# Optimization experiments

Measured on AMD Instinct MI355X. Metric: run time of the kernel, lower is better.

Reference implementation:

```python
import jax, jax.numpy as jnp
import numpy as np

D = 64       # hidden_dim
ED = 16      # edge_dim
N = 50000
E = 400000
T = 2
STEP = 0.5   # euler fixed step over t in [0,1] -> 2 steps
EPS = 1e-5

def setup_inputs() -> dict:
    key = jax.random.key(0)
    ks = jax.random.split(key, 14)
    def lin(k, fi, fo):
        return jax.random.normal(k, (fi, fo), jnp.float32) / np.sqrt(fi)
    return {
        'h_seq': jax.random.normal(ks[0], (T, N, D), jnp.float32),
        'edge_attr': jax.random.normal(ks[1], (T, E, ED), jnp.float32),
        # msg_net: MLP(2D+ED -> D -> D), 2 layers with ReLU
        'W1': lin(ks[2], 2 * D + ED, D), 'b1': jnp.zeros((D,), jnp.float32),
        'W2': lin(ks[3], D, D),          'b2': jnp.zeros((D,), jnp.float32),
        # dynamics_net: Linear(2D,D) -> LayerNorm -> SiLU -> Linear(D,D) -> Tanh
        'Wd1': lin(ks[4], 2 * D, D), 'bd1': jnp.zeros((D,), jnp.float32),
        'ln_g': jnp.ones((D,), jnp.float32), 'ln_b': jnp.zeros((D,), jnp.float32),
        'Wd2': lin(ks[5], D, D), 'bd2': jnp.zeros((D,), jnp.float32),
        'edge_index': jax.random.randint(ks[6], (T, 2, E), 0, N, jnp.int32),
    }

def _ode_func(h, row, col, ea, W1, b1, W2, b2, Wd1, bd1, ln_g, ln_b, Wd2, bd2):
    # identity transport: Q_uv @ h_v == h_v
    h_transported = h[col]                              # [E, D]
    msg_in = jnp.concatenate([h[row], h_transported, ea], axis=-1)  # [E, 2D+ED]
    msg = jax.nn.relu(msg_in @ W1 + b1) @ W2 + b2       # [E, D]
    agg = jax.ops.segment_sum(msg, row, num_segments=h.shape[0])    # [N, D]
    x = jnp.concatenate([h, agg], axis=-1) @ Wd1 + bd1  # [N, D]
    mu = x.mean(-1, keepdims=True)
    var = x.var(-1, keepdims=True)
    x = (x - mu) * jax.lax.rsqrt(var + EPS) * ln_g + ln_b
    x = jax.nn.silu(x) @ Wd2 + bd2
    return jnp.tanh(x)

def reference(h_seq, edge_attr, W1, b1, W2, b2, Wd1, bd1, ln_g, ln_b, Wd2, bd2, edge_index):
    params = (W1, b1, W2, b2, Wd1, bd1, ln_g, ln_b, Wd2, bd2)
    n_steps = int(round(1.0 / STEP))
    h_prev = h_seq[0]
    disagreements = []
    for t in range(T):
        row, col = edge_index[t, 0], edge_index[t, 1]
        ea = edge_attr[t]
        h = h_prev + h_seq[t]                           # h_fused
        for _ in range(n_steps):                        # fixed-step Euler
            h = h + STEP * _ode_func(h, row, col, ea, *params)
        diff = h[row] - h[col]                          # Q=I -> h_u - h_v
        disagreements.append(jnp.minimum((diff * diff).sum(-1), 1e4))
        h_prev = h
    return h_prev, jnp.stack(disagreements)             # h_final [N,D], D [T,E]
```

## Files before the change

kernel.cpp:

```cpp
#include <hip/hip_runtime.h>

#define NN 50000
#define EE 400000
#define NT64 6250
#define EGRID 1250
#define NBLK 782
#define SBLK 49

typedef __bf16 bf16x8 __attribute__((ext_vector_type(8)));
typedef float f32x4 __attribute__((ext_vector_type(4)));

static __device__ __forceinline__ ushort f2bf(float f) {
    union { float f; unsigned int i; } x; x.f = f;
    unsigned int r = x.i + 0x7fffu + ((x.i >> 16) & 1u);
    return (ushort)(r >> 16);
}
static __device__ __forceinline__ float bf2f(ushort u) {
    union { unsigned int i; float f; } x; x.i = ((unsigned int)u) << 16; return x.f;
}
static __device__ __forceinline__ unsigned pack2(float lo, float hi) {
    return (unsigned)f2bf(lo) | ((unsigned)f2bf(hi) << 16);
}
static __device__ __forceinline__ float fast_tanh(float x) {
    float e = __expf(2.f * x);
    return 1.f - 2.f / (e + 1.f);
}
static __device__ __forceinline__ bf16x8 pk8(float4 f0, float4 f1) {
    union { uint4 u; bf16x8 v; } z;
    z.u = make_uint4(pack2(f0.x, f0.y), pack2(f0.z, f0.w),
                     pack2(f1.x, f1.y), pack2(f1.z, f1.w));
    return z.v;
}
static __device__ __forceinline__ bf16x8 zero8() {
    union { uint4 u; bf16x8 v; } z;
    z.u = make_uint4(0u, 0u, 0u, 0u);
    return z.v;
}

__global__ __launch_bounds__(256) void prep_edge_k(
    const float* __restrict__ W1, const float* __restrict__ W2,
    const float* __restrict__ b1, const float* __restrict__ b2,
    ushort* __restrict__ B1P, ushort* __restrict__ B2P,
    float* __restrict__ b1f, float* __restrict__ b2f)
{
    int idx = blockIdx.x * 256 + threadIdx.x;
    if (idx < 10240) {
        int j = idx & 7, n = (idx >> 3) & 63, qk = idx >> 9;
        int kc = qk >> 2, quad = qk & 3;
        int k = kc * 32 + quad * 8 + j;
        B1P[idx] = (k < 144) ? f2bf(W1[k * 64 + n]) : (ushort)0;
    }
    if (idx < 4096) {
        int j = idx & 7, n = (idx >> 3) & 63, qk = idx >> 9;
        int kc = qk >> 2, quad = qk & 3;
        int k = kc * 32 + quad * 8 + j;
        B2P[idx] = f2bf(W2[k * 64 + n]);
    }
    if (idx < 64) { b1f[idx] = b1[idx]; b2f[idx] = b2[idx]; }
}

__global__ __launch_bounds__(256) void prep_node_k(
    const float* __restrict__ Wd1, const float* __restrict__ Wd2,
    const float* __restrict__ bd1, const float* __restrict__ lng,
    const float* __restrict__ lnb, const float* __restrict__ bd2,
    ushort* __restrict__ Wd1P, ushort* __restrict__ Wd2P,
    float* __restrict__ bd1f, float* __restrict__ lngf,
    float* __restrict__ lnbf, float* __restrict__ bd2f)
{
    int idx = blockIdx.x * 256 + threadIdx.x;
    if (idx < 8192) {
        int j = idx & 7, n = (idx >> 3) & 63, qk = idx >> 9;
        int kc = qk >> 2, quad = qk & 3;
        int k = kc * 32 + quad * 8 + j;
        Wd1P[idx] = f2bf(Wd1[k * 64 + n]);
    }
    if (idx < 4096) {
        int j = idx & 7, n = (idx >> 3) & 63, qk = idx >> 9;
        int kc = qk >> 2, quad = qk & 3;
        int k = kc * 32 + quad * 8 + j;
        Wd2P[idx] = f2bf(Wd2[k * 64 + n]);
    }
    if (idx < 64) {
        bd1f[idx] = bd1[idx]; lngf[idx] = lng[idx];
        lnbf[idx] = lnb[idx]; bd2f[idx] = bd2[idx];
    }
}

__global__ __launch_bounds__(256) void state_k(
    float* __restrict__ h, ushort* __restrict__ hb,
    const float* __restrict__ hseq_t, int mode)
{
    int i = blockIdx.x * 256 + threadIdx.x;
    float v = hseq_t[i];
    float r = (mode == 0) ? (2.f * v) : (h[i] + v);
    h[i] = r; hb[i] = f2bf(r);
}

__global__ __launch_bounds__(256) void zero_k(int* __restrict__ p, int n) {
    int i = blockIdx.x * 256 + threadIdx.x;
    if (i < n) p[i] = 0;
}
__global__ __launch_bounds__(256) void zero_f(float* __restrict__ p) {
    int i = blockIdx.x * 256 + threadIdx.x;
    p[i] = 0.f;
}
__global__ __launch_bounds__(256) void hist_k(const int* __restrict__ rows, int* __restrict__ counts) {
    int e = blockIdx.x * 256 + threadIdx.x;
    if (e < EE) atomicAdd(&counts[rows[e]], 1);
}

__global__ __launch_bounds__(256) void scanA_k(
    const int* __restrict__ counts, int* __restrict__ offsets, int* __restrict__ bsum)
{
    __shared__ int wsum[4];
    int tid = threadIdx.x, lane = tid & 63, w = tid >> 6;
    int i4 = blockIdx.x * 1024 + tid * 4;
    int4 v = make_int4(0, 0, 0, 0);
    if (i4 + 3 < NN) v = *(const int4*)(counts + i4);
    else {
        if (i4 < NN) v.x = counts[i4];
        if (i4 + 1 < NN) v.y = counts[i4 + 1];
        if (i4 + 2 < NN) v.z = counts[i4 + 2];
    }
    int s = v.x + v.y + v.z + v.w;
    int x = s;
    for (int off = 1; off < 64; off <<= 1) {
        int y = __shfl_up(x, off);
        if (lane >= off) x += y;
    }
    if (lane == 63) wsum[w] = x;
    __syncthreads();
    int wpre = 0;
    for (int j = 0; j < w; j++) wpre += wsum[j];
    int excl = wpre + x - s;
    int e0 = excl, e1 = e0 + v.x, e2 = e1 + v.y, e3 = e2 + v.z;
    if (i4 + 3 < NN) *(int4*)(offsets + i4) = make_int4(e0, e1, e2, e3);
    else {
        if (i4 < NN) offsets[i4] = e0;
        if (i4 + 1 < NN) offsets[i4 + 1] = e1;
        if (i4 + 2 < NN) offsets[i4 + 2] = e2;
    }
    if (tid == 255) bsum[blockIdx.x] = wpre + x;
}
__global__ __launch_bounds__(256) void scanC_k(
    const int* __restrict__ offsets, const int* __restrict__ bsum, int* __restrict__ cursor)
{
    int i = blockIdx.x * 256 + threadIdx.x;
    if (i < NN) {
        int b = i >> 10;
        int add = 0;
        for (int j = 0; j < b; j++) add += bsum[j];
        cursor[i] = offsets[i] + add;
    }
}

__global__ __launch_bounds__(256) void fill_idx_k(
    const int* __restrict__ rows, int* __restrict__ cursor, int* __restrict__ esort)
{
    int e = blockIdx.x * 256 + threadIdx.x;
    if (e < EE) {
        int p = atomicAdd(&cursor[rows[e]], 1);
        if ((unsigned)p < (unsigned)EE) esort[p] = e;
    }
}

__global__ __launch_bounds__(256) void gather_k(
    const int* __restrict__ esort, const int* __restrict__ rows,
    const int* __restrict__ cols, const float* __restrict__ ea,
    int* __restrict__ rsort, int* __restrict__ csort, ushort* __restrict__ eab)
{
    int p = blockIdx.x * 256 + threadIdx.x;
    if (p < EE) {
        int e = esort[p];
        rsort[p] = rows[e];
        csort[p] = cols[e];
        const float* sp = ea + (size_t)e * 16;
        float4 f0 = ((const float4*)sp)[0], f1 = ((const float4*)sp)[1];
        float4 f2 = ((const float4*)sp)[2], f3 = ((const float4*)sp)[3];
        uint4* dp = (uint4*)(eab + (size_t)p * 16);
        dp[0] = make_uint4(pack2(f0.x, f0.y), pack2(f0.z, f0.w),
                           pack2(f1.x, f1.y), pack2(f1.z, f1.w));
        dp[1] = make_uint4(pack2(f2.x, f2.y), pack2(f2.z, f2.w),
                           pack2(f3.x, f3.y), pack2(f3.z, f3.w));
    }
}

template<int MODE>
__global__ __launch_bounds__(256, 5) void edge_k(
    const ushort* __restrict__ hb,
    const int* __restrict__ ridx, const int* __restrict__ cidx,
    const ushort* __restrict__ eab, const float* __restrict__ eaf,
    const ushort* __restrict__ B1P, const ushort* __restrict__ B2P,
    const float* __restrict__ b1f, const float* __restrict__ b2f,
    float* __restrict__ agg)
{
    __shared__ __attribute__((aligned(16))) ushort sB1[10240];
    __shared__ __attribute__((aligned(16))) ushort sH[64 * 72];

    int tid = threadIdx.x;
    int lane = tid & 63, wave = tid >> 6;
    int m = lane & 15, quad = lane >> 4;

    for (int i = tid; i < 10240 / 8; i += 256) ((uint4*)sB1)[i] = ((const uint4*)B1P)[i];
    bf16x8 b2r[2][4];
    for (int kc = 0; kc < 2; kc++)
        for (int nt = 0; nt < 4; nt++)
            b2r[kc][nt] = *(const bf16x8*)(B2P + ((kc * 4 + quad) * 64 + nt * 16 + m) * 8);
    float b1v[4], b2v[4];
    for (int nt = 0; nt < 4; nt++) { b1v[nt] = b1f[nt * 16 + m]; b2v[nt] = b2f[nt * 16 + m]; }
    __syncthreads();

    ushort* sHw = sH + wave * 1152;
    int sl = wave * 16 + m;

    int t0 = blockIdx.x * 5;
    int r_n = ridx[t0 * 64 + sl], c_n = cidx[t0 * 64 + sl];

    for (int t = t0; t < t0 + 5; t++) {
        int s = t * 64 + sl;
        int r = r_n, c = c_n;

        bf16x8 a[5];
        a[0] = *(const bf16x8*)(hb + (size_t)r * 64 + quad * 8);
        a[1] = *(const bf16x8*)(hb + (size_t)r * 64 + 32 + quad * 8);
        a[2] = *(const bf16x8*)(hb + (size_t)c * 64 + quad * 8);
        a[3] = *(const bf16x8*)(hb + (size_t)c * 64 + 32 + quad * 8);
        a[4] = zero8();
        if (MODE == 0) {
            if (quad < 2) a[4] = *(const bf16x8*)(eab + (size_t)s * 16 + quad * 8);
        } else {
            if (quad < 2) {
                const float* sp = eaf + (size_t)s * 16 + quad * 8;
                float4 f0 = ((const float4*)sp)[0], f1 = ((const float4*)sp)[1];
                a[4] = pk8(f0, f1);
            }
        }

        int tn = t + 1; if (tn >= t0 + 5) tn = t;
        int sn = tn * 64 + sl;
        r_n = ridx[sn]; c_n = cidx[sn];

        f32x4 acc[4];
        #pragma unroll
        for (int nt = 0; nt < 4; nt++) acc[nt] = (f32x4){0.f, 0.f, 0.f, 0.f};
        #pragma unroll
        for (int kc = 0; kc < 5; kc++) {
            #pragma unroll
            for (int nt = 0; nt < 4; nt++) {
                bf16x8 b = *(const bf16x8*)(sB1 + ((kc * 4 + quad) * 64 + nt * 16 + m) * 8);
                acc[nt] = __builtin_amdgcn_mfma_f32_16x16x32_bf16(a[kc], b, acc[nt], 0, 0, 0);
            }
        }

        __builtin_amdgcn_wave_barrier();
        #pragma unroll
        for (int nt = 0; nt < 4; nt++) {
            int colid = nt * 16 + m;
            float bb = b1v[nt];
            #pragma unroll
            for (int rr = 0; rr < 4; rr++) {
                float v = acc[nt][rr] + bb;
                v = v > 0.f ? v : 0.f;
                sHw[(quad * 4 + rr) * 72 + colid] = f2bf(v);
            }
        }
        __builtin_amdgcn_wave_barrier();

        f32x4 acc2[4];
        #pragma unroll
        for (int nt = 0; nt < 4; nt++) acc2[nt] = (f32x4){0.f, 0.f, 0.f, 0.f};
        #pragma unroll
        for (int kc = 0; kc < 2; kc++) {
            bf16x8 av = *(const bf16x8*)(sHw + m * 72 + kc * 32 + quad * 8);
            #pragma unroll
            for (int nt = 0; nt < 4; nt++) {
                acc2[nt] = __builtin_amdgcn_mfma_f32_16x16x32_bf16(av, b2r[kc][nt], acc2[nt], 0, 0, 0);
            }
        }

        int base = t * 64 + wave * 16 + quad * 4;
        int r0 = ridx[base], r1 = ridx[base + 1], r2 = ridx[base + 2], r3 = ridx[base + 3];
        #pragma unroll
        for (int nt = 0; nt < 4; nt++) {
            int colid = nt * 16 + m;
            float bb = b2v[nt];
            float v0 = acc2[nt][0] + bb, v1 = acc2[nt][1] + bb;
            float v2 = acc2[nt][2] + bb, v3 = acc2[nt][3] + bb;
            float sum = v0; int pr = r0;
            if (r1 == pr) sum += v1;
            else { atomicAdd(&agg[(size_t)pr * 64 + colid], sum); pr = r1; sum = v1; }
            if (r2 == pr) sum += v2;
            else { atomicAdd(&agg[(size_t)pr * 64 + colid], sum); pr = r2; sum = v2; }
            if (r3 == pr) sum += v3;
            else { atomicAdd(&agg[(size_t)pr * 64 + colid], sum); pr = r3; sum = v3; }
            atomicAdd(&agg[(size_t)pr * 64 + colid], sum);
        }
    }
}

__global__ __launch_bounds__(256, 4) void node_k(
    float* __restrict__ h, ushort* __restrict__ hbm,
    float* __restrict__ agg,
    const ushort* __restrict__ Wd1P, const ushort* __restrict__ Wd2P,
    const float* __restrict__ bd1f, const float* __restrict__ lngf,
    const float* __restrict__ lnbf, const float* __restrict__ bd2f)
{
    __shared__ __attribute__((aligned(16))) ushort sB1[8192];
    __shared__ __attribute__((aligned(16))) ushort sB2[4096];
    __shared__ __attribute__((aligned(16))) ushort sX[64 * 72];
    int tid = threadIdx.x;
    int lane = tid & 63, wave = tid >> 6;
    int m = lane & 15, quad = lane >> 4;
    int nbase = blockIdx.x * 64;

    for (int i = tid; i < 8192 / 8; i += 256) ((uint4*)sB1)[i] = ((const uint4*)Wd1P)[i];
    for (int i = tid; i < 4096 / 8; i += 256) ((uint4*)sB2)[i] = ((const uint4*)Wd2P)[i];
    float gA[4], bA[4], d1[4], d2[4];
    for (int nt = 0; nt < 4; nt++) {
        int f = nt * 16 + m;
        d1[nt] = bd1f[f]; gA[nt] = lngf[f]; bA[nt] = lnbf[f]; d2[nt] = bd2f[f];
    }
    __syncthreads();

    int n_true = nbase + wave * 16 + m;
    bool own = (n_true < NN);
    int n = own ? n_true : (NN - 1);
    bf16x8 A[4];
    A[0] = *(const bf16x8*)(hbm + (size_t)n * 64 + quad * 8);
    A[1] = *(const bf16x8*)(hbm + (size_t)n * 64 + 32 + quad * 8);
    {
        const float* ap = agg + (size_t)n * 64 + quad * 8;
        float4 g0 = ((const float4*)ap)[0], g1 = ((const float4*)ap)[1];
        const float* ap2 = agg + (size_t)n * 64 + 32 + quad * 8;
        float4 g2 = ((const float4*)ap2)[0], g3 = ((const float4*)ap2)[1];
        A[2] = pk8(g0, g1);
        A[3] = pk8(g2, g3);
        if (own) {
            float4 z = make_float4(0.f, 0.f, 0.f, 0.f);
            ((float4*)(agg + (size_t)n * 64 + quad * 8))[0] = z;
            ((float4*)(agg + (size_t)n * 64 + quad * 8))[1] = z;
            ((float4*)(agg + (size_t)n * 64 + 32 + quad * 8))[0] = z;
            ((float4*)(agg + (size_t)n * 64 + 32 + quad * 8))[1] = z;
        }
    }

    f32x4 acc[4];
    #pragma unroll
    for (int nt = 0; nt < 4; nt++) acc[nt] = (f32x4){0.f, 0.f, 0.f, 0.f};
    #pragma unroll
    for (int kc = 0; kc < 4; kc++) {
        #pragma unroll
        for (int nt = 0; nt < 4; nt++) {
            bf16x8 b = *(const bf16x8*)(sB1 + ((kc * 4 + quad) * 64 + nt * 16 + m) * 8);
            acc[nt] = __builtin_amdgcn_mfma_f32_16x16x32_bf16(A[kc], b, acc[nt], 0, 0, 0);
        }
    }

    float xs[4][4];
    #pragma unroll
    for (int nt = 0; nt < 4; nt++)
        #pragma unroll
        for (int r = 0; r < 4; r++)
            xs[nt][r] = acc[nt][r] + d1[nt];

    ushort* sXw = sX + wave * 1152;
    #pragma unroll
    for (int r = 0; r < 4; r++) {
        float s1 = 0.f, s2 = 0.f;
        #pragma unroll
        for (int nt = 0; nt < 4; nt++) { float v = xs[nt][r]; s1 += v; s2 += v * v; }
        for (int off = 1; off < 16; off <<= 1) {
            s1 += __shfl_xor(s1, off);
            s2 += __shfl_xor(s2, off);
        }
        float mean = s1 * (1.f / 64.f);
        float var = fmaxf(s2 * (1.f / 64.f) - mean * mean, 0.f);
        float rstd = rsqrtf(var + 1e-5f);
        #pragma unroll
        for (int nt = 0; nt < 4; nt++) {
            float xn = (xs[nt][r] - mean) * rstd * gA[nt] + bA[nt];
            float sl = xn / (1.f + __expf(-xn));
            sXw[(quad * 4 + r) * 72 + nt * 16 + m] = f2bf(sl);
        }
    }
    __builtin_amdgcn_wave_barrier();

    f32x4 acc2[4];
    #pragma unroll
    for (int nt = 0; nt < 4; nt++) acc2[nt] = (f32x4){0.f, 0.f, 0.f, 0.f};
    #pragma unroll
    for (int kc = 0; kc < 2; kc++) {
        bf16x8 av = *(const bf16x8*)(sXw + m * 72 + kc * 32 + quad * 8);
        #pragma unroll
        for (int nt = 0; nt < 4; nt++) {
            bf16x8 b = *(const bf16x8*)(sB2 + ((kc * 4 + quad) * 64 + nt * 16 + m) * 8);
            acc2[nt] = __builtin_amdgcn_mfma_f32_16x16x32_bf16(av, b, acc2[nt], 0, 0, 0);
        }
    }

    #pragma unroll
    for (int r = 0; r < 4; r++) {
        int g = nbase + wave * 16 + quad * 4 + r;
        if (g < NN) {
            #pragma unroll
            for (int nt = 0; nt < 4; nt++) {
                int f = nt * 16 + m;
                float y = fast_tanh(acc2[nt][r] + d2[nt]);
                float hn = h[(size_t)g * 64 + f] + 0.5f * y;
                h[(size_t)g * 64 + f] = hn;
                hbm[(size_t)g * 64 + f] = f2bf(hn);
            }
        }
    }
}

__global__ __launch_bounds__(256) void dis_k(
    const float* __restrict__ h, const int* __restrict__ rows,
    const int* __restrict__ cols, float* __restrict__ outp)
{
    int tid = threadIdx.x;
    int e = blockIdx.x * 16 + (tid >> 4);
    int l16 = tid & 15;
    int r = rows[e], c = cols[e];
    float4 a = *(const float4*)(h + (size_t)r * 64 + l16 * 4);
    float4 b = *(const float4*)(h + (size_t)c * 64 + l16 * 4);
    float dx = a.x - b.x, dy = a.y - b.y, dz = a.z - b.z, dw = a.w - b.w;
    float s = dx * dx + dy * dy + dz * dz + dw * dw;
    for (int off = 1; off < 16; off <<= 1) s += __shfl_xor(s, off);
    if (l16 == 0) outp[e] = (s < 1e4f ? s : 1e4f);
}

__global__ __launch_bounds__(256) void final_k(const float* __restrict__ h, float* __restrict__ out) {
    int i = blockIdx.x * 256 + threadIdx.x;
    out[i] = h[i];
}

extern "C" void kernel_launch(void* const* d_in, const int* in_sizes, int n_in,
                              void* d_out, int out_size, void* d_ws, size_t ws_size,
                              hipStream_t stream) {
    const float* h_seq = (const float*)d_in[0];
    const float* eattr = (const float*)d_in[1];
    const float* W1 = (const float*)d_in[2];
    const float* b1 = (const float*)d_in[3];
    const float* W2 = (const float*)d_in[4];
    const float* b2 = (const float*)d_in[5];
    const float* Wd1 = (const float*)d_in[6];
    const float* bd1 = (const float*)d_in[7];
    const float* lng = (const float*)d_in[8];
    const float* lnb = (const float*)d_in[9];
    const float* Wd2 = (const float*)d_in[10];
    const float* bd2 = (const float*)d_in[11];
    const int* ei = (const int*)d_in[12];
    float* out = (float*)d_out;

    char* wsp = (char*)d_ws;
    size_t used = 0;
    auto carve = [&](size_t b) {
        void* p = (void*)(wsp + used);
        used += (b + 255) & ~(size_t)255;
        return p;
    };
    float* h      = (float*)carve((size_t)NN * 64 * 4);
    ushort* hb    = (ushort*)carve((size_t)NN * 64 * 2);
    float* agg    = (float*)carve((size_t)NN * 64 * 4);
    ushort* B1P   = (ushort*)carve(10240 * 2);
    ushort* B2P   = (ushort*)carve(4096 * 2);
    ushort* Wd1P  = (ushort*)carve(8192 * 2);
    ushort* Wd2P  = (ushort*)carve(4096 * 2);
    float* b1f    = (float*)carve(256);
    float* b2f    = (float*)carve(256);
    float* bd1f   = (float*)carve(256);
    float* lngf   = (float*)carve(256);
    float* lnbf   = (float*)carve(256);
    float* bd2f   = (float*)carve(256);
    int* counts   = (int*)carve((size_t)NN * 4);
    int* offsets  = (int*)carve((size_t)(NN + 1) * 4);
    int* cursor   = (int*)carve((size_t)NN * 4);
    int* bsum     = (int*)carve(256);
    int* esort    = (int*)carve((size_t)EE * 4);
    int* rsort    = (int*)carve((size_t)EE * 4);
    int* csort    = (int*)carve((size_t)EE * 4);
    ushort* eab   = (ushort*)carve((size_t)EE * 16 * 2);
    const bool full = (used <= ws_size);

    zero_f<<<12500, 256, 0, stream>>>(agg);
    prep_edge_k<<<40, 256, 0, stream>>>(W1, W2, b1, b2, B1P, B2P, b1f, b2f);
    prep_node_k<<<32, 256, 0, stream>>>(Wd1, Wd2, bd1, lng, lnb, bd2, Wd1P, Wd2P, bd1f, lngf, lnbf, bd2f);

    for (int t = 0; t < 2; t++) {
        const int* rows = ei + (size_t)t * 2 * EE;
        const int* cols = rows + EE;
        const float* eat = eattr + (size_t)t * EE * 16;
        state_k<<<12500, 256, 0, stream>>>(h, hb, h_seq + (size_t)t * NN * 64, t);
        if (full) {
            zero_k<<<196, 256, 0, stream>>>(counts, NN);
            hist_k<<<1563, 256, 0, stream>>>(rows, counts);
            scanA_k<<<SBLK, 256, 0, stream>>>(counts, offsets, bsum);
            scanC_k<<<196, 256, 0, stream>>>(offsets, bsum, cursor);
            fill_idx_k<<<1563, 256, 0, stream>>>(rows, cursor, esort);
            gather_k<<<1563, 256, 0, stream>>>(esort, rows, cols, eat, rsort, csort, eab);
        }
        for (int s = 0; s < 2; s++) {
            if (full) {
                edge_k<0><<<EGRID, 256, 0, stream>>>(hb, rsort, csort, eab, (const float*)0,
                                                     B1P, B2P, b1f, b2f, agg);
            } else {
                edge_k<1><<<EGRID, 256, 0, stream>>>(hb, rows, cols, (const ushort*)0, eat,
                                                     B1P, B2P, b1f, b2f, agg);
            }
            node_k<<<NBLK, 256, 0, stream>>>(h, hb, agg, Wd1P, Wd2P,
                                             bd1f, lngf, lnbf, bd2f);
        }
        dis_k<<<25000, 256, 0, stream>>>(h, rows, cols, out + (size_t)NN * 64 + (size_t)t * EE);
    }
    final_k<<<12500, 256, 0, stream>>>(h, out);
}
```

Measured before the change: 659.1 us.

## Fuse edge message, segment aggregation and node update into one per-node-block kernel

Replaces the separate edge kernel (global float atomics into agg) and node kernel with a single kernel where each block owns 64 destination nodes. It walks that block's row-sorted CSR edge range, accumulates messages in shared memory with LDS atomics, then runs the dynamics MLP, LayerNorm and tanh update in place. The h state is ping-ponged between two buffers so that reading old h while writing new h stays correct. This removes the global agg zeroing, global atomics and the agg round-trip. The cost is per-block load imbalance from uneven degree, lower occupancy (launch bounds 3) and loss of the prefetch of the next edge indices.

```diff
diff --git a/kernel.cpp b/kernel.cpp
--- a/kernel.cpp
+++ b/kernel.cpp
@@ -143,15 +143,17 @@
     if (tid == 255) bsum[blockIdx.x] = wpre + x;
 }
 __global__ __launch_bounds__(256) void scanC_k(
-    const int* __restrict__ offsets, const int* __restrict__ bsum, int* __restrict__ cursor)
+    int* __restrict__ offsets, const int* __restrict__ bsum, int* __restrict__ cursor)
 {
     int i = blockIdx.x * 256 + threadIdx.x;
     if (i < NN) {
         int b = i >> 10;
         int add = 0;
         for (int j = 0; j < b; j++) add += bsum[j];
-        cursor[i] = offsets[i] + add;
-    }
+        int o = offsets[i] + add;
+        offsets[i] = o; cursor[i] = o;
+    }
+    if (i == 0) offsets[NN] = EE;
 }
 
 __global__ __launch_bounds__(256) void fill_idx_k(
@@ -185,11 +187,214 @@
     }
 }
 
-template<int MODE>
-__global__ __launch_bounds__(256, 5) void edge_k(
+__global__ __launch_bounds__(256, 3) void mega_k(
+    const float* __restrict__ hin, const ushort* __restrict__ hbin,
+    float* __restrict__ hout, ushort* __restrict__ hbout,
+    const int* __restrict__ offsets,
+    const int* __restrict__ rsort, const int* __restrict__ csort,
+    const ushort* __restrict__ eab,
+    const ushort* __restrict__ B1P, const ushort* __restrict__ B2P,
+    const float* __restrict__ b1f, const float* __restrict__ b2f,
+    const ushort* __restrict__ Wd1P, const ushort* __restrict__ Wd2P,
+    const float* __restrict__ bd1f, const float* __restrict__ lngf,
+    const float* __restrict__ lnbf, const float* __restrict__ bd2f)
+{
+    __shared__ __attribute__((aligned(16))) ushort sB1[10240];
+    __shared__ __attribute__((aligned(16))) float aggL[65][68];
+    __shared__ __attribute__((aligned(16))) ushort sHX[64 * 72];
+
+    int tid = threadIdx.x;
+    int lane = tid & 63, wave = tid >> 6;
+    int m = lane & 15, quad = lane >> 4;
+    int nbase = blockIdx.x * 64;
+    int nb_end = nbase + 64; if (nb_end > NN) nb_end = NN;
+    int beg = offsets[nbase], end = offsets[nb_end];
+
+    for (int i = tid; i < 10240 / 8; i += 256) ((uint4*)sB1)[i] = ((const uint4*)B1P)[i];
+    {
+        float* af = &aggL[0][0];
+        for (int i = tid; i < 65 * 68; i += 256) af[i] = 0.f;
+    }
+    bf16x8 b2r[2][4];
+    for (int kc = 0; kc < 2; kc++)
+        for (int nt = 0; nt < 4; nt++)
+            b2r[kc][nt] = *(const bf16x8*)(B2P + ((kc * 4 + quad) * 64 + nt * 16 + m) * 8);
+    float b1v[4], b2v[4], gA[4], bA[4], d1[4], d2[4];
+    for (int nt = 0; nt < 4; nt++) {
+        int f = nt * 16 + m;
+        b1v[nt] = b1f[f]; b2v[nt] = b2f[f];
+        d1[nt] = bd1f[f]; gA[nt] = lngf[f]; bA[nt] = lnbf[f]; d2[nt] = bd2f[f];
+    }
+    __syncthreads();
+
+    ushort* sHw = sHX + wave * 1152;
+    int sl = wave * 16 + m;
+    int ntile = (end - beg + 63) >> 6;
+
+    for (int t = 0; t < ntile; t++) {
+        int sb = beg + t * 64;
+        int s = sb + sl;
+        int sload = s < end ? s : end - 1;
+        int r = rsort[sload], c = csort[sload];
+
+        bf16x8 a[5];
+        a[0] = *(const bf16x8*)(hbin + (size_t)r * 64 + quad * 8);
+        a[1] = *(const bf16x8*)(hbin + (size_t)r * 64 + 32 + quad * 8);
+        a[2] = *(const bf16x8*)(hbin + (size_t)c * 64 + quad * 8);
+        a[3] = *(const bf16x8*)(hbin + (size_t)c * 64 + 32 + quad * 8);
+        a[4] = zero8();
+        if (quad < 2) a[4] = *(const bf16x8*)(eab + (size_t)sload * 16 + quad * 8);
+
+        f32x4 acc[4];
+        #pragma unroll
+        for (int nt = 0; nt < 4; nt++) acc[nt] = (f32x4){0.f, 0.f, 0.f, 0.f};
+        #pragma unroll
+        for (int kc = 0; kc < 5; kc++) {
+            #pragma unroll
+            for (int nt = 0; nt < 4; nt++) {
+                bf16x8 b = *(const bf16x8*)(sB1 + ((kc * 4 + quad) * 64 + nt * 16 + m) * 8);
+                acc[nt] = __builtin_amdgcn_mfma_f32_16x16x32_bf16(a[kc], b, acc[nt], 0, 0, 0);
+            }
+        }
+
+        __builtin_amdgcn_wave_barrier();
+        #pragma unroll
+        for (int nt = 0; nt < 4; nt++) {
+            int colid = nt * 16 + m;
+            float bb = b1v[nt];
+            #pragma unroll
+            for (int rr = 0; rr < 4; rr++) {
+                float v = acc[nt][rr] + bb;
+                v = v > 0.f ? v : 0.f;
+                sHw[(quad * 4 + rr) * 72 + colid] = f2bf(v);
+            }
+        }
+        __builtin_amdgcn_wave_barrier();
+
+        f32x4 acc2[4];
+        #pragma unroll
+        for (int nt = 0; nt < 4; nt++) acc2[nt] = (f32x4){0.f, 0.f, 0.f, 0.f};
+        #pragma unroll
+        for (int kc = 0; kc < 2; kc++) {
+            bf16x8 av = *(const bf16x8*)(sHw + m * 72 + kc * 32 + quad * 8);
+            #pragma unroll
+            for (int nt = 0; nt < 4; nt++) {
+                acc2[nt] = __builtin_amdgcn_mfma_f32_16x16x32_bf16(av, b2r[kc][nt], acc2[nt], 0, 0, 0);
+            }
+        }
+
+        int gb = sb + wave * 16 + quad * 4;
+        int l0 = (gb     < end) ? rsort[gb]     - nbase : 64;
+        int l1 = (gb + 1 < end) ? rsort[gb + 1] - nbase : 64;
+        int l2 = (gb + 2 < end) ? rsort[gb + 2] - nbase : 64;
+        int l3 = (gb + 3 < end) ? rsort[gb + 3] - nbase : 64;
+        #pragma unroll
+        for (int nt = 0; nt < 4; nt++) {
+            int colid = nt * 16 + m;
+            float bb = b2v[nt];
+            float v0 = acc2[nt][0] + bb, v1 = acc2[nt][1] + bb;
+            float v2 = acc2[nt][2] + bb, v3 = acc2[nt][3] + bb;
+            float sum = v0; int pr = l0;
+            if (l1 == pr) sum += v1;
+            else { atomicAdd(&aggL[pr][colid], sum); pr = l1; sum = v1; }
+            if (l2 == pr) sum += v2;
+            else { atomicAdd(&aggL[pr][colid], sum); pr = l2; sum = v2; }
+            if (l3 == pr) sum += v3;
+            else { atomicAdd(&aggL[pr][colid], sum); pr = l3; sum = v3; }
+            atomicAdd(&aggL[pr][colid], sum);
+        }
+    }
+    __syncthreads();
+
+    int n_true = nbase + wave * 16 + m;
+    bool own = (n_true < NN);
+    int n = own ? n_true : (NN - 1);
+    bf16x8 A[4];
+    A[0] = *(const bf16x8*)(hbin + (size_t)n * 64 + quad * 8);
+    A[1] = *(const bf16x8*)(hbin + (size_t)n * 64 + 32 + quad * 8);
+    {
+        int nl = wave * 16 + m;
+        float4 g0 = *(const float4*)&aggL[nl][quad * 8];
+        float4 g1 = *(const float4*)&aggL[nl][quad * 8 + 4];
+        float4 g2 = *(const float4*)&aggL[nl][32 + quad * 8];
+        float4 g3 = *(const float4*)&aggL[nl][32 + quad * 8 + 4];
+        A[2] = pk8(g0, g1);
+        A[3] = pk8(g2, g3);
+    }
+
+    f32x4 acc[4];
+    #pragma unroll
+    for (int nt = 0; nt < 4; nt++) acc[nt] = (f32x4){0.f, 0.f, 0.f, 0.f};
+    #pragma unroll
+    for (int kc = 0; kc < 4; kc++) {
+        #pragma unroll
+        for (int nt = 0; nt < 4; nt++) {
+            bf16x8 b = *(const bf16x8*)(Wd1P + ((kc * 4 + quad) * 64 + nt * 16 + m) * 8);
+            acc[nt] = __builtin_amdgcn_mfma_f32_16x16x32_bf16(A[kc], b, acc[nt], 0, 0, 0);
+        }
+    }
+
+    float xs[4][4];
+    #pragma unroll
+    for (int nt = 0; nt < 4; nt++)
+        #pragma unroll
+        for (int r = 0; r < 4; r++)
+            xs[nt][r] = acc[nt][r] + d1[nt];
+
+    #pragma unroll
+    for (int r = 0; r < 4; r++) {
+        float s1 = 0.f, s2 = 0.f;
+        #pragma unroll
+        for (int nt = 0; nt < 4; nt++) { float v = xs[nt][r]; s1 += v; s2 += v * v; }
+        for (int off = 1; off < 16; off <<= 1) {
+            s1 += __shfl_xor(s1, off);
+            s2 += __shfl_xor(s2, off);
+        }
+        float mean = s1 * (1.f / 64.f);
+        float var = fmaxf(s2 * (1.f / 64.f) - mean * mean, 0.f);
+        float rstd = rsqrtf(var + 1e-5f);
+        #pragma unroll
+        for (int nt = 0; nt < 4; nt++) {
+            float xn = (xs[nt][r] - mean) * rstd * gA[nt] + bA[nt];
+            float slv = xn / (1.f + __expf(-xn));
+            sHw[(quad * 4 + r) * 72 + nt * 16 + m] = f2bf(slv);
+        }
+    }
+    __builtin_amdgcn_wave_barrier();
+
+    f32x4 acc2[4];
+    #pragma unroll
+    for (int nt = 0; nt < 4; nt++) acc2[nt] = (f32x4){0.f, 0.f, 0.f, 0.f};
+    #pragma unroll
+    for (int kc = 0; kc < 2; kc++) {
+        bf16x8 av = *(const bf16x8*)(sHw + m * 72 + kc * 32 + quad * 8);
+        #pragma unroll
+        for (int nt = 0; nt < 4; nt++) {
+            bf16x8 b = *(const bf16x8*)(Wd2P + ((kc * 4 + quad) * 64 + nt * 16 + m) * 8);
+            acc2[nt] = __builtin_amdgcn_mfma_f32_16x16x32_bf16(av, b, acc2[nt], 0, 0, 0);
+        }
+    }
+
+    #pragma unroll
+    for (int r = 0; r < 4; r++) {
+        int g = nbase + wave * 16 + quad * 4 + r;
+        if (g < NN) {
+            #pragma unroll
+            for (int nt = 0; nt < 4; nt++) {
+                int f = nt * 16 + m;
+                float y = fast_tanh(acc2[nt][r] + d2[nt]);
+                float hn = hin[(size_t)g * 64 + f] + 0.5f * y;
+                hout[(size_t)g * 64 + f] = hn;
+                hbout[(size_t)g * 64 + f] = f2bf(hn);
+            }
+        }
+    }
+}
+
+__global__ __launch_bounds__(256, 5) void edge_fb_k(
     const ushort* __restrict__ hb,
     const int* __restrict__ ridx, const int* __restrict__ cidx,
-    const ushort* __restrict__ eab, const float* __restrict__ eaf,
+    const float* __restrict__ eaf,
     const ushort* __restrict__ B1P, const ushort* __restrict__ B2P,
     const float* __restrict__ b1f, const float* __restrict__ b2f,
     float* __restrict__ agg)
@@ -212,60 +417,43 @@
 
     ushort* sHw = sH + wave * 1152;
     int sl = wave * 16 + m;
-
     int t0 = blockIdx.x * 5;
-    int r_n = ridx[t0 * 64 + sl], c_n = cidx[t0 * 64 + sl];
 
     for (int t = t0; t < t0 + 5; t++) {
         int s = t * 64 + sl;
-        int r = r_n, c = c_n;
-
+        int r = ridx[s], c = cidx[s];
         bf16x8 a[5];
         a[0] = *(const bf16x8*)(hb + (size_t)r * 64 + quad * 8);
         a[1] = *(const bf16x8*)(hb + (size_t)r * 64 + 32 + quad * 8);
         a[2] = *(const bf16x8*)(hb + (size_t)c * 64 + quad * 8);
         a[3] = *(const bf16x8*)(hb + (size_t)c * 64 + 32 + quad * 8);
         a[4] = zero8();
-        if (MODE == 0) {
-            if (quad < 2) a[4] = *(const bf16x8*)(eab + (size_t)s * 16 + quad * 8);
-        } else {
-            if (quad < 2) {
-                const float* sp = eaf + (size_t)s * 16 + quad * 8;
-                float4 f0 = ((const float4*)sp)[0], f1 = ((const float4*)sp)[1];
-                a[4] = pk8(f0, f1);
-            }
-        }
-
-        int tn = t + 1; if (tn >= t0 + 5) tn = t;
-        int sn = tn * 64 + sl;
-        r_n = ridx[sn]; c_n = cidx[sn];
-
+        if (quad < 2) {
+            const float* sp = eaf + (size_t)s * 16 + quad * 8;
+            a[4] = pk8(((const float4*)sp)[0], ((const float4*)sp)[1]);
+        }
         f32x4 acc[4];
         #pragma unroll
         for (int nt = 0; nt < 4; nt++) acc[nt] = (f32x4){0.f, 0.f, 0.f, 0.f};
         #pragma unroll
-        for (int kc = 0; kc < 5; kc++) {
+        for (int kc = 0; kc < 5; kc++)
             #pragma unroll
             for (int nt = 0; nt < 4; nt++) {
                 bf16x8 b = *(const bf16x8*)(sB1 + ((kc * 4 + quad) * 64 + nt * 16 + m) * 8);
                 acc[nt] = __builtin_amdgcn_mfma_f32_16x16x32_bf16(a[kc], b, acc[nt], 0, 0, 0);
             }
-        }
-
         __builtin_amdgcn_wave_barrier();
         #pragma unroll
         for (int nt = 0; nt < 4; nt++) {
-            int colid = nt * 16 + m;
             float bb = b1v[nt];
             #pragma unroll
             for (int rr = 0; rr < 4; rr++) {
                 float v = acc[nt][rr] + bb;
                 v = v > 0.f ? v : 0.f;
-                sHw[(quad * 4 + rr) * 72 + colid] = f2bf(v);
+                sHw[(quad * 4 + rr) * 72 + nt * 16 + m] = f2bf(v);
             }
         }
         __builtin_amdgcn_wave_barrier();
-
         f32x4 acc2[4];
         #pragma unroll
         for (int nt = 0; nt < 4; nt++) acc2[nt] = (f32x4){0.f, 0.f, 0.f, 0.f};
@@ -273,11 +461,9 @@
         for (int kc = 0; kc < 2; kc++) {
             bf16x8 av = *(const bf16x8*)(sHw + m * 72 + kc * 32 + quad * 8);
             #pragma unroll
-            for (int nt = 0; nt < 4; nt++) {
+            for (int nt = 0; nt < 4; nt++)
                 acc2[nt] = __builtin_amdgcn_mfma_f32_16x16x32_bf16(av, b2r[kc][nt], acc2[nt], 0, 0, 0);
-            }
-        }
-
+        }
         int base = t * 64 + wave * 16 + quad * 4;
         int r0 = ridx[base], r1 = ridx[base + 1], r2 = ridx[base + 2], r3 = ridx[base + 3];
         #pragma unroll
@@ -348,13 +534,12 @@
     #pragma unroll
     for (int nt = 0; nt < 4; nt++) acc[nt] = (f32x4){0.f, 0.f, 0.f, 0.f};
     #pragma unroll
-    for (int kc = 0; kc < 4; kc++) {
+    for (int kc = 0; kc < 4; kc++)
         #pragma unroll
         for (int nt = 0; nt < 4; nt++) {
             bf16x8 b = *(const bf16x8*)(sB1 + ((kc * 4 + quad) * 64 + nt * 16 + m) * 8);
             acc[nt] = __builtin_amdgcn_mfma_f32_16x16x32_bf16(A[kc], b, acc[nt], 0, 0, 0);
         }
-    }
 
     float xs[4][4];
     #pragma unroll
@@ -379,8 +564,8 @@
         #pragma unroll
         for (int nt = 0; nt < 4; nt++) {
             float xn = (xs[nt][r] - mean) * rstd * gA[nt] + bA[nt];
-            float sl = xn / (1.f + __expf(-xn));
-            sXw[(quad * 4 + r) * 72 + nt * 16 + m] = f2bf(sl);
+            float slv = xn / (1.f + __expf(-xn));
+            sXw[(quad * 4 + r) * 72 + nt * 16 + m] = f2bf(slv);
         }
     }
     __builtin_amdgcn_wave_barrier();
@@ -460,8 +645,10 @@
         used += (b + 255) & ~(size_t)255;
         return p;
     };
-    float* h      = (float*)carve((size_t)NN * 64 * 4);
-    ushort* hb    = (ushort*)carve((size_t)NN * 64 * 2);
+    float* h0     = (float*)carve((size_t)NN * 64 * 4);
+    ushort* hb0   = (ushort*)carve((size_t)NN * 64 * 2);
+    float* h1     = (float*)carve((size_t)NN * 64 * 4);
+    ushort* hb1   = (ushort*)carve((size_t)NN * 64 * 2);
     float* agg    = (float*)carve((size_t)NN * 64 * 4);
     ushort* B1P   = (ushort*)carve(10240 * 2);
     ushort* B2P   = (ushort*)carve(4096 * 2);
@@ -483,15 +670,15 @@
     ushort* eab   = (ushort*)carve((size_t)EE * 16 * 2);
     const bool full = (used <= ws_size);
 
-    zero_f<<<12500, 256, 0, stream>>>(agg);
     prep_edge_k<<<40, 256, 0, stream>>>(W1, W2, b1, b2, B1P, B2P, b1f, b2f);
     prep_node_k<<<32, 256, 0, stream>>>(Wd1, Wd2, bd1, lng, lnb, bd2, Wd1P, Wd2P, bd1f, lngf, lnbf, bd2f);
+    if (!full) zero_f<<<12500, 256, 0, stream>>>(agg);
 
     for (int t = 0; t < 2; t++) {
         const int* rows = ei + (size_t)t * 2 * EE;
         const int* cols = rows + EE;
         const float* eat = eattr + (size_t)t * EE * 16;
-        state_k<<<12500, 256, 0, stream>>>(h, hb, h_seq + (size_t)t * NN * 64, t);
+        state_k<<<12500, 256, 0, stream>>>(h0, hb0, h_seq + (size_t)t * NN * 64, t);
         if (full) {
             zero_k<<<196, 256, 0, stream>>>(counts, NN);
             hist_k<<<1563, 256, 0, stream>>>(rows, counts);
@@ -499,19 +686,21 @@
             scanC_k<<<196, 256, 0, stream>>>(offsets, bsum, cursor);
             fill_idx_k<<<1563, 256, 0, stream>>>(rows, cursor, esort);
             gather_k<<<1563, 256, 0, stream>>>(esort, rows, cols, eat, rsort, csort, eab);
-        }
-        for (int s = 0; s < 2; s++) {
-            if (full) {
-                edge_k<0><<<EGRID, 256, 0, stream>>>(hb, rsort, csort, eab, (const float*)0,
+            mega_k<<<NBLK, 256, 0, stream>>>(h0, hb0, h1, hb1, offsets, rsort, csort, eab,
+                                             B1P, B2P, b1f, b2f, Wd1P, Wd2P,
+                                             bd1f, lngf, lnbf, bd2f);
+            mega_k<<<NBLK, 256, 0, stream>>>(h1, hb1, h0, hb0, offsets, rsort, csort, eab,
+                                             B1P, B2P, b1f, b2f, Wd1P, Wd2P,
+                                             bd1f, lngf, lnbf, bd2f);
+        } else {
+            for (int s = 0; s < 2; s++) {
+                edge_fb_k<<<EGRID, 256, 0, stream>>>(hb0, rows, cols, eat,
                                                      B1P, B2P, b1f, b2f, agg);
-            } else {
-                edge_k<1><<<EGRID, 256, 0, stream>>>(hb, rows, cols, (const ushort*)0, eat,
-                                                     B1P, B2P, b1f, b2f, agg);
+                node_k<<<NBLK, 256, 0, stream>>>(h0, hb0, agg, Wd1P, Wd2P,
+                                                 bd1f, lngf, lnbf, bd2f);
             }
-            node_k<<<NBLK, 256, 0, stream>>>(h, hb, agg, Wd1P, Wd2P,
-                                             bd1f, lngf, lnbf, bd2f);
-        }
-        dis_k<<<25000, 256, 0, stream>>>(h, rows, cols, out + (size_t)NN * 64 + (size_t)t * EE);
-    }
-    final_k<<<12500, 256, 0, stream>>>(h, out);
-}
+        }
+        dis_k<<<25000, 256, 0, stream>>>(h0, rows, cols, out + (size_t)NN * 64 + (size_t)t * EE);
+    }
+    final_k<<<12500, 256, 0, stream>>>(h0, out);
+}
```

Result: slower. 705.3 us (+7.0%).
